# Performance work log

Measured on AMD Instinct MI355X. Metric: run time of the kernel, lower is better.

Reference implementation:

```python
import jax, jax.numpy as jnp
import numpy as np
from jax import lax

DN = ('NHWC', 'HWIO', 'NHWC')

def _conv(x, w):
    return lax.conv_general_dilated(x, w, window_strides=(1, 1), padding='SAME', dimension_numbers=DN)

def _hard_sigmoid(z):
    # keras hard_sigmoid: clip(0.2*z + 0.5, 0, 1) -- default recurrent_activation of ConvLSTM2D
    return jnp.clip(0.2 * z + 0.5, 0.0, 1.0)

def setup_inputs() -> dict:
    key = jax.random.key(0)
    ks = jax.random.split(key, 6)
    B, T, H, W, Cin = 4, 16, 64, 64, 32
    F, kh, kw = 64, 3, 3
    x  = jax.random.normal(ks[0], (B, T, H, W, Cin), dtype=jnp.float32)
    Wx = jax.random.normal(ks[1], (kh, kw, Cin, 4 * F), dtype=jnp.float32) * 0.05
    Wh = jax.random.normal(ks[2], (kh, kw, F, 4 * F), dtype=jnp.float32) * 0.05
    b  = jnp.zeros((4 * F,), dtype=jnp.float32)
    Wp = jax.random.normal(ks[3], (1, 1, Cin, F), dtype=jnp.float32) * 0.05
    bp = jnp.zeros((F,), dtype=jnp.float32)
    return {"x": x, "Wx": Wx, "Wh": Wh, "b": b, "Wp": Wp, "bp": bp}

def reference(x, Wx, Wh, b, Wp, bp):
    B, T, H, W, Cin = x.shape
    F = Wh.shape[2]
    # Precompute the input-to-gate convolutions for all timesteps at once.
    zx = _conv(x.reshape(B * T, H, W, Cin), Wx) + b          # (B*T, H, W, 4F)
    zx = zx.reshape(B, T, H, W, 4 * F).transpose(1, 0, 2, 3, 4)  # time-major

    def step(carry, zx_t):
        h, c = carry
        z = zx_t + _conv(h, Wh)                              # (B, H, W, 4F)
        zi, zf, zc, zo = jnp.split(z, 4, axis=-1)            # keras gate order i,f,c,o
        i = _hard_sigmoid(zi)
        f = _hard_sigmoid(zf)
        c_new = f * c + i * jnp.tanh(zc)
        o = _hard_sigmoid(zo)
        h_new = o * jnp.tanh(c_new)
        return (h_new, c_new), h_new

    h0 = jnp.zeros((B, H, W, F), dtype=x.dtype)
    c0 = jnp.zeros((B, H, W, F), dtype=x.dtype)
    _, hs = lax.scan(step, (h0, c0), zx)                     # (T, B, H, W, F)
    convlstm_out = hs.transpose(1, 0, 2, 3, 4)               # (B, T, H, W, F)

    # TimeDistributed 1x1 projection of the input as the residual branch.
    residual = _conv(x.reshape(B * T, H, W, Cin), Wp) + bp
    residual = residual.reshape(B, T, H, W, F)
    return convlstm_out + residual
```

## Files before the change

kernel.cpp:

```cpp
#include <hip/hip_runtime.h>

#define B_ 4
#define T_ 16
#define H_ 64
#define W_ 64
#define CIN 32
#define F_ 64
#define NCH 256
#define KSTEPS 27
#define TSLAB (H_ * W_ * F_)

#define OFF_H0 557056
#define OFF_H1 2654208

typedef __attribute__((ext_vector_type(8))) short short8;
typedef __attribute__((ext_vector_type(4))) float floatx4;
typedef __attribute__((address_space(3))) unsigned int  lds_u32;
typedef __attribute__((address_space(1))) const unsigned int g_u32;

__device__ __forceinline__ unsigned short f2bf(float f) {
  union { float f; unsigned u; } v; v.f = f;
  unsigned r = v.u + 0x7FFFu + ((v.u >> 16) & 1u);
  return (unsigned short)(r >> 16);
}

__device__ __forceinline__ float tanh_fast(float z) {
  float e = __expf(2.0f * z);
  return 1.0f - 2.0f * __builtin_amdgcn_rcpf(e + 1.0f);
}

__global__ void prep_weights(const float* __restrict__ Wx, const float* __restrict__ Wh,
                             unsigned short* __restrict__ WT) {
  int idx = blockIdx.x * 256 + threadIdx.x;
  int s = idx / 10240;
  int r = idx - s * 10240;
  int n = r / 40;
  int c = r - n * 40;
  unsigned short v = 0;
  if (c < 32) {
    int k  = s * 32 + c;
    int g  = k / 96;
    int ch = k - g * 96;
    float f = (ch < CIN) ? Wx[(g * CIN + ch) * NCH + n]
                         : Wh[(g * F_ + (ch - CIN)) * NCH + n];
    v = f2bf(f);
  }
  WT[idx] = v;
}

__global__ void prep_zero_h(float4* __restrict__ p) {
  int idx = blockIdx.x * 256 + threadIdx.x;
  p[idx] = make_float4(0.f, 0.f, 0.f, 0.f);
}

__global__ void prep_zero_c(float* __restrict__ out) {
  int idx = blockIdx.x * 256 + threadIdx.x;
  int b = idx >> 16;
  int i = idx & 65535;
  ((float4*)(out + (size_t)b * (T_ * TSLAB)))[i] = make_float4(0.f, 0.f, 0.f, 0.f);
}

__device__ __forceinline__ void stage_wt(const unsigned short* __restrict__ src,
                                         short* dstbuf, int w, int lane) {
  __attribute__((address_space(3))) unsigned short* d =
      (__attribute__((address_space(3))) unsigned short*)dstbuf + w * 2560;
  const unsigned short* s = src + w * 2560 + lane * 8;
  #pragma unroll
  for (int q = 0; q < 5; q++)
    __builtin_amdgcn_global_load_lds((g_u32*)(s + q * 512), (lds_u32*)(d + q * 512),
                                     16, 0, 0);
}

__global__ __launch_bounds__(256, 1)
void step_kernel(const float* __restrict__ x, const float* __restrict__ bias,
                 const float* __restrict__ Wp, const float* __restrict__ bp,
                 const unsigned short* __restrict__ WT,
                 const unsigned short* __restrict__ hprev,
                 unsigned short* __restrict__ hnew,
                 float* __restrict__ out, int t)
{
  __shared__ __align__(16) char smem[77824];
  short* patch = (short*)smem;
  short* bl0   = (short*)(smem + 28288);
  short* bl1   = (short*)(smem + 48768);
  float* gact  = (float*)smem;
  float* WpL   = (float*)(smem + 69632);

  const int tid  = threadIdx.x;
  const int w    = tid >> 6;
  const int lane = tid & 63;
  const int quad = lane >> 4;
  const int lr   = lane & 15;

  const int bid = blockIdx.x;
  const int b   = bid >> 6;
  const int rem = bid & 63;
  const int y0  = (rem >> 1) << 1;
  const int x0  = (rem & 1) << 5;

  stage_wt(WT, bl0, w, lane);

  if (tid < 136) {
    int sy = tid / 34, sx = tid - sy * 34;
    int yy = y0 + sy - 1, xx = x0 + sx - 1;
    short* dst = patch + tid * 104;
    if (yy >= 0 && yy < H_ && xx >= 0 && xx < W_) {
      const float4* xs = (const float4*)(x + ((((b * T_ + t) * H_ + yy) * W_ + xx) * CIN));
      #pragma unroll
      for (int j = 0; j < 4; j++) {
        float4 f0 = xs[2 * j];
        float4 f1 = xs[2 * j + 1];
        union { short8 v; unsigned short u[8]; } pk;
        pk.u[0] = f2bf(f0.x); pk.u[1] = f2bf(f0.y); pk.u[2] = f2bf(f0.z); pk.u[3] = f2bf(f0.w);
        pk.u[4] = f2bf(f1.x); pk.u[5] = f2bf(f1.y); pk.u[6] = f2bf(f1.z); pk.u[7] = f2bf(f1.w);
        ((short8*)dst)[j] = pk.v;
      }
      const uint4* hs = (const uint4*)(hprev + ((b * H_ + yy) * W_ + xx) * F_);
      uint4* d2 = (uint4*)(dst + 32);
      #pragma unroll
      for (int j = 0; j < 8; j++) d2[j] = hs[j];
    } else {
      uint4 z = make_uint4(0, 0, 0, 0);
      uint4* d4 = (uint4*)dst;
      #pragma unroll
      for (int j = 0; j < 12; j++) d4[j] = z;
    }
  }

  float bias_r[4];
  #pragma unroll
  for (int nf = 0; nf < 4; nf++) bias_r[nf] = bias[w * 64 + nf * 16 + lr];

  floatx4 acc[4][4];
  #pragma unroll
  for (int mf = 0; mf < 4; mf++)
    #pragma unroll
    for (int nf = 0; nf < 4; nf++)
      acc[mf][nf] = (floatx4){0.f, 0.f, 0.f, 0.f};

  __syncthreads();

  const unsigned short* wsrc = WT + 10240;
  for (int s = 0; s < KSTEPS; s++) {
    short* cur = (s & 1) ? bl1 : bl0;
    if (s < KSTEPS - 1) {
      stage_wt(wsrc, (s & 1) ? bl0 : bl1, w, lane);
      wsrc += 10240;
    }
    int g  = s / 3;
    int c0 = (s - g * 3) * 32;
    int dy = g / 3, dx = g - dy * 3;
    short8 afr[4], bfr[4];
    #pragma unroll
    for (int mf = 0; mf < 4; mf++) {
      int p  = mf * 16 + lr;
      int ty = p >> 5, tx = p & 31;
      afr[mf] = *(const short8*)(patch + ((ty + dy) * 34 + tx + dx) * 104 + c0 + quad * 8);
    }
    #pragma unroll
    for (int nf = 0; nf < 4; nf++) {
      int n = w * 64 + nf * 16 + lr;
      bfr[nf] = *(const short8*)(cur + n * 40 + quad * 8);
    }
    #pragma unroll
    for (int mf = 0; mf < 4; mf++)
      #pragma unroll
      for (int nf = 0; nf < 4; nf++)
        acc[mf][nf] = __builtin_amdgcn_mfma_f32_16x16x32_bf16(afr[mf], bfr[nf], acc[mf][nf], 0, 0, 0);
    __syncthreads();
  }

  #pragma unroll
  for (int mf = 0; mf < 4; mf++)
    #pragma unroll
    for (int nf = 0; nf < 4; nf++)
      #pragma unroll
      for (int r = 0; r < 4; r++) {
        int mm = mf * 16 + quad * 4 + r;
        float z = acc[mf][nf][r] + bias_r[nf];
        float a;
        if (w == 2) a = tanh_fast(z);
        else {
          a = __builtin_fmaf(z, 0.2f, 0.5f);
          a = fminf(fmaxf(a, 0.f), 1.f);
        }
        gact[(w * 64 + mm) * 68 + nf * 16 + lr] = a;
      }
  {
    float4* d = (float4*)WpL;
    const float4* sWp = (const float4*)Wp;
    d[tid * 2]     = sWp[tid * 2];
    d[tid * 2 + 1] = sWp[tid * 2 + 1];
  }

  const int mloc = tid >> 2;
  const int cb   = (tid & 3) * 16;
  const int tyo  = mloc >> 5, txo = mloc & 31;
  const int gy   = y0 + tyo, gx = x0 + txo;
  const int hbase   = ((b * H_ + gy) * W_ + gx) * F_ + cb;
  const int outbase = (((b * T_ + t) * H_ + gy) * W_ + gx) * F_ + cb;

  float xv[32];
  {
    const float4* xs = (const float4*)(x + ((((b * T_ + t) * H_ + gy) * W_ + gx) * CIN));
    #pragma unroll
    for (int j = 0; j < 8; j++) {
      float4 f = xs[j];
      xv[4 * j] = f.x; xv[4 * j + 1] = f.y; xv[4 * j + 2] = f.z; xv[4 * j + 3] = f.w;
    }
  }
  float4 co4[4];
  #pragma unroll
  for (int j = 0; j < 4; j++) co4[j] = *(const float4*)(out + outbase + 4 * j);

  __syncthreads();

  float res[16];
  #pragma unroll
  for (int j = 0; j < 16; j++) res[j] = bp[cb + j];
  for (int ci = 0; ci < 32; ci++) {
    float xf = xv[ci];
    #pragma unroll
    for (int j4 = 0; j4 < 4; j4++) {
      float4 wv = *(const float4*)(WpL + ci * 64 + cb + j4 * 4);
      res[j4 * 4 + 0] += xf * wv.x;
      res[j4 * 4 + 1] += xf * wv.y;
      res[j4 * 4 + 2] += xf * wv.z;
      res[j4 * 4 + 3] += xf * wv.w;
    }
  }

  union { unsigned short hv[16]; uint4 q[2]; } hu;
  #pragma unroll
  for (int j4 = 0; j4 < 4; j4++) {
    int jj = j4 * 4;
    float4 gi = *(const float4*)(gact + (0 * 64 + mloc) * 68 + cb + jj);
    float4 gf = *(const float4*)(gact + (1 * 64 + mloc) * 68 + cb + jj);
    float4 gg = *(const float4*)(gact + (2 * 64 + mloc) * 68 + cb + jj);
    float4 go = *(const float4*)(gact + (3 * 64 + mloc) * 68 + cb + jj);
    float cold[4] = {co4[j4].x, co4[j4].y, co4[j4].z, co4[j4].w};
    float iv[4] = {gi.x, gi.y, gi.z, gi.w};
    float fv[4] = {gf.x, gf.y, gf.z, gf.w};
    float gv[4] = {gg.x, gg.y, gg.z, gg.w};
    float ov[4] = {go.x, go.y, go.z, go.w};
    float cn4[4], h4[4];
    #pragma unroll
    for (int e = 0; e < 4; e++) {
      float cn = fv[e] * cold[e] + iv[e] * gv[e];
      float h  = ov[e] * tanh_fast(cn);
      cn4[e] = cn; h4[e] = h;
      hu.hv[jj + e] = f2bf(h);
    }
    if (t < T_ - 1)
      *(float4*)(out + outbase + TSLAB + jj) = make_float4(cn4[0], cn4[1], cn4[2], cn4[3]);
    *(float4*)(out + outbase + jj) = make_float4(h4[0] + res[jj + 0], h4[1] + res[jj + 1],
                                                 h4[2] + res[jj + 2], h4[3] + res[jj + 3]);
  }
  uint4* hd = (uint4*)(hnew + hbase);
  hd[0] = hu.q[0];
  hd[1] = hu.q[1];
}

extern "C" void kernel_launch(void* const* d_in, const int* in_sizes, int n_in,
                              void* d_out, int out_size, void* d_ws, size_t ws_size,
                              hipStream_t stream) {
  const float* x    = (const float*)d_in[0];
  const float* Wx   = (const float*)d_in[1];
  const float* Wh   = (const float*)d_in[2];
  const float* bias = (const float*)d_in[3];
  const float* Wp   = (const float*)d_in[4];
  const float* bp   = (const float*)d_in[5];
  float* out = (float*)d_out;

  unsigned short* WT = (unsigned short*)d_ws;
  unsigned short* h0 = (unsigned short*)((char*)d_ws + OFF_H0);
  unsigned short* h1 = (unsigned short*)((char*)d_ws + OFF_H1);

  hipLaunchKernelGGL(prep_weights, dim3(1080), dim3(256), 0, stream, Wx, Wh, WT);
  hipLaunchKernelGGL(prep_zero_h, dim3(1024), dim3(256), 0, stream,
                     (float4*)((char*)d_ws + OFF_H0));
  hipLaunchKernelGGL(prep_zero_c, dim3(1024), dim3(256), 0, stream, out);

  for (int t = 0; t < T_; t++) {
    const unsigned short* hp = (t & 1) ? h1 : h0;
    unsigned short*       hn = (t & 1) ? h0 : h1;
    hipLaunchKernelGGL(step_kernel, dim3(256), dim3(256), 0, stream,
                       x, bias, Wp, bp, WT, hp, hn, out, t);
  }
}
```

Before: 711.2 us.

## Halve per-block tile to one row and launch twice as many blocks

Each block now covers a 1x32 pixel tile instead of 2x32, so the grid doubles to 512 blocks. This fills more of the GPU's compute units and allows two blocks per CU through smaller LDS use and launch_bounds(256,2). The gate-activation buffer is transposed and the epilogue thread mapping is reworked to handle 8 channels per thread. Each block still stages the full weight set, so total weight traffic doubles and halo overhead per output pixel grows.

```diff
diff --git a/kernel.cpp b/kernel.cpp
--- a/kernel.cpp
+++ b/kernel.cpp
@@ -71,7 +71,7 @@
                                      16, 0, 0);
 }
 
-__global__ __launch_bounds__(256, 1)
+__global__ __launch_bounds__(256, 2)
 void step_kernel(const float* __restrict__ x, const float* __restrict__ bias,
                  const float* __restrict__ Wp, const float* __restrict__ bp,
                  const unsigned short* __restrict__ WT,
@@ -79,12 +79,12 @@
                  unsigned short* __restrict__ hnew,
                  float* __restrict__ out, int t)
 {
-  __shared__ __align__(16) char smem[77824];
+  __shared__ __align__(16) char smem[62176];
   short* patch = (short*)smem;
-  short* bl0   = (short*)(smem + 28288);
-  short* bl1   = (short*)(smem + 48768);
+  short* bl0   = (short*)(smem + 21216);
+  short* bl1   = (short*)(smem + 41696);
   float* gact  = (float*)smem;
-  float* WpL   = (float*)(smem + 69632);
+  float* WpL   = (float*)(smem + 49152);
 
   const int tid  = threadIdx.x;
   const int w    = tid >> 6;
@@ -93,14 +93,14 @@
   const int lr   = lane & 15;
 
   const int bid = blockIdx.x;
-  const int b   = bid >> 6;
-  const int rem = bid & 63;
-  const int y0  = (rem >> 1) << 1;
+  const int b   = bid >> 7;
+  const int rem = bid & 127;
+  const int y0  = rem >> 1;
   const int x0  = (rem & 1) << 5;
 
   stage_wt(WT, bl0, w, lane);
 
-  if (tid < 136) {
+  if (tid < 102) {
     int sy = tid / 34, sx = tid - sy * 34;
     int yy = y0 + sy - 1, xx = x0 + sx - 1;
     short* dst = patch + tid * 104;
@@ -131,9 +131,9 @@
   #pragma unroll
   for (int nf = 0; nf < 4; nf++) bias_r[nf] = bias[w * 64 + nf * 16 + lr];
 
-  floatx4 acc[4][4];
-  #pragma unroll
-  for (int mf = 0; mf < 4; mf++)
+  floatx4 acc[2][4];
+  #pragma unroll
+  for (int mf = 0; mf < 2; mf++)
     #pragma unroll
     for (int nf = 0; nf < 4; nf++)
       acc[mf][nf] = (floatx4){0.f, 0.f, 0.f, 0.f};
@@ -150,12 +150,11 @@
     int g  = s / 3;
     int c0 = (s - g * 3) * 32;
     int dy = g / 3, dx = g - dy * 3;
-    short8 afr[4], bfr[4];
-    #pragma unroll
-    for (int mf = 0; mf < 4; mf++) {
-      int p  = mf * 16 + lr;
-      int ty = p >> 5, tx = p & 31;
-      afr[mf] = *(const short8*)(patch + ((ty + dy) * 34 + tx + dx) * 104 + c0 + quad * 8);
+    short8 afr[2], bfr[4];
+    #pragma unroll
+    for (int mf = 0; mf < 2; mf++) {
+      int tx = mf * 16 + lr;
+      afr[mf] = *(const short8*)(patch + (dy * 34 + tx + dx) * 104 + c0 + quad * 8);
     }
     #pragma unroll
     for (int nf = 0; nf < 4; nf++) {
@@ -163,7 +162,7 @@
       bfr[nf] = *(const short8*)(cur + n * 40 + quad * 8);
     }
     #pragma unroll
-    for (int mf = 0; mf < 4; mf++)
+    for (int mf = 0; mf < 2; mf++)
       #pragma unroll
       for (int nf = 0; nf < 4; nf++)
         acc[mf][nf] = __builtin_amdgcn_mfma_f32_16x16x32_bf16(afr[mf], bfr[nf], acc[mf][nf], 0, 0, 0);
@@ -171,12 +170,12 @@
   }
 
   #pragma unroll
-  for (int mf = 0; mf < 4; mf++)
+  for (int mf = 0; mf < 2; mf++)
     #pragma unroll
     for (int nf = 0; nf < 4; nf++)
       #pragma unroll
       for (int r = 0; r < 4; r++) {
-        int mm = mf * 16 + quad * 4 + r;
+        int p = mf * 16 + quad * 4 + r;
         float z = acc[mf][nf][r] + bias_r[nf];
         float a;
         if (w == 2) a = tanh_fast(z);
@@ -184,7 +183,7 @@
           a = __builtin_fmaf(z, 0.2f, 0.5f);
           a = fminf(fmaxf(a, 0.f), 1.f);
         }
-        gact[(w * 64 + mm) * 68 + nf * 16 + lr] = a;
+        gact[(w * 64 + nf * 16 + lr) * 37 + p] = a;
       }
   {
     float4* d = (float4*)WpL;
@@ -193,10 +192,9 @@
     d[tid * 2 + 1] = sWp[tid * 2 + 1];
   }
 
-  const int mloc = tid >> 2;
-  const int cb   = (tid & 3) * 16;
-  const int tyo  = mloc >> 5, txo = mloc & 31;
-  const int gy   = y0 + tyo, gx = x0 + txo;
+  const int mloc = tid >> 3;
+  const int cb   = (tid & 7) * 8;
+  const int gy   = y0, gx = x0 + mloc;
   const int hbase   = ((b * H_ + gy) * W_ + gx) * F_ + cb;
   const int outbase = (((b * T_ + t) * H_ + gy) * W_ + gx) * F_ + cb;
 
@@ -209,19 +207,19 @@
       xv[4 * j] = f.x; xv[4 * j + 1] = f.y; xv[4 * j + 2] = f.z; xv[4 * j + 3] = f.w;
     }
   }
-  float4 co4[4];
-  #pragma unroll
-  for (int j = 0; j < 4; j++) co4[j] = *(const float4*)(out + outbase + 4 * j);
+  float4 co4[2];
+  #pragma unroll
+  for (int j = 0; j < 2; j++) co4[j] = *(const float4*)(out + outbase + 4 * j);
 
   __syncthreads();
 
-  float res[16];
-  #pragma unroll
-  for (int j = 0; j < 16; j++) res[j] = bp[cb + j];
+  float res[8];
+  #pragma unroll
+  for (int j = 0; j < 8; j++) res[j] = bp[cb + j];
   for (int ci = 0; ci < 32; ci++) {
     float xf = xv[ci];
     #pragma unroll
-    for (int j4 = 0; j4 < 4; j4++) {
+    for (int j4 = 0; j4 < 2; j4++) {
       float4 wv = *(const float4*)(WpL + ci * 64 + cb + j4 * 4);
       res[j4 * 4 + 0] += xf * wv.x;
       res[j4 * 4 + 1] += xf * wv.y;
@@ -230,35 +228,34 @@
     }
   }
 
-  union { unsigned short hv[16]; uint4 q[2]; } hu;
-  #pragma unroll
-  for (int j4 = 0; j4 < 4; j4++) {
-    int jj = j4 * 4;
-    float4 gi = *(const float4*)(gact + (0 * 64 + mloc) * 68 + cb + jj);
-    float4 gf = *(const float4*)(gact + (1 * 64 + mloc) * 68 + cb + jj);
-    float4 gg = *(const float4*)(gact + (2 * 64 + mloc) * 68 + cb + jj);
-    float4 go = *(const float4*)(gact + (3 * 64 + mloc) * 68 + cb + jj);
-    float cold[4] = {co4[j4].x, co4[j4].y, co4[j4].z, co4[j4].w};
-    float iv[4] = {gi.x, gi.y, gi.z, gi.w};
-    float fv[4] = {gf.x, gf.y, gf.z, gf.w};
-    float gv[4] = {gg.x, gg.y, gg.z, gg.w};
-    float ov[4] = {go.x, go.y, go.z, go.w};
+  float iv[8], fv[8], gv[8], ov[8];
+  #pragma unroll
+  for (int j = 0; j < 8; j++) {
+    iv[j] = gact[(0 * 64 + cb + j) * 37 + mloc];
+    fv[j] = gact[(1 * 64 + cb + j) * 37 + mloc];
+    gv[j] = gact[(2 * 64 + cb + j) * 37 + mloc];
+    ov[j] = gact[(3 * 64 + cb + j) * 37 + mloc];
+  }
+  union { unsigned short hv[8]; uint4 q; } hu;
+  #pragma unroll
+  for (int j4 = 0; j4 < 2; j4++) {
+    float cold[4] = {j4 ? co4[1].x : co4[0].x, j4 ? co4[1].y : co4[0].y,
+                     j4 ? co4[1].z : co4[0].z, j4 ? co4[1].w : co4[0].w};
     float cn4[4], h4[4];
     #pragma unroll
     for (int e = 0; e < 4; e++) {
-      float cn = fv[e] * cold[e] + iv[e] * gv[e];
-      float h  = ov[e] * tanh_fast(cn);
+      int j = j4 * 4 + e;
+      float cn = fv[j] * cold[e] + iv[j] * gv[j];
+      float h  = ov[j] * tanh_fast(cn);
       cn4[e] = cn; h4[e] = h;
-      hu.hv[jj + e] = f2bf(h);
+      hu.hv[j] = f2bf(h);
     }
     if (t < T_ - 1)
-      *(float4*)(out + outbase + TSLAB + jj) = make_float4(cn4[0], cn4[1], cn4[2], cn4[3]);
-    *(float4*)(out + outbase + jj) = make_float4(h4[0] + res[jj + 0], h4[1] + res[jj + 1],
-                                                 h4[2] + res[jj + 2], h4[3] + res[jj + 3]);
-  }
-  uint4* hd = (uint4*)(hnew + hbase);
-  hd[0] = hu.q[0];
-  hd[1] = hu.q[1];
+      *(float4*)(out + outbase + TSLAB + j4 * 4) = make_float4(cn4[0], cn4[1], cn4[2], cn4[3]);
+    *(float4*)(out + outbase + j4 * 4) = make_float4(h4[0] + res[j4 * 4 + 0], h4[1] + res[j4 * 4 + 1],
+                                                     h4[2] + res[j4 * 4 + 2], h4[3] + res[j4 * 4 + 3]);
+  }
+  *(uint4*)(hnew + hbase) = hu.q;
 }
 
 extern "C" void kernel_launch(void* const* d_in, const int* in_sizes, int n_in,
@@ -284,7 +281,7 @@
   for (int t = 0; t < T_; t++) {
     const unsigned short* hp = (t & 1) ? h1 : h0;
     unsigned short*       hn = (t & 1) ? h0 : h1;
-    hipLaunchKernelGGL(step_kernel, dim3(256), dim3(256), 0, stream,
+    hipLaunchKernelGGL(step_kernel, dim3(512), dim3(256), 0, stream,
                        x, bias, Wp, bp, WT, hp, hn, out, t);
   }
 }
```

Result: slower. 780.9 us (+9.8%).
